# Kernel tuning notes

Measured on AMD Instinct MI355X. Metric: run time of the kernel, lower is better.

## Reference

```python
import jax, jax.numpy as jnp
import numpy as np

SIDE_LEN = 128
RESOLUTION = 1.0  # Angstrom per pixel


def setup_inputs() -> dict:
    key = jax.random.key(0)
    k1, k2, k3 = jax.random.split(key, 3)
    B, A = 16, 20000
    # atom xyz coords in Angstrom, spread within the field of view (+/- 63.5 A)
    mol = jax.random.normal(k1, (B, A, 3), dtype=jnp.float32) * 20.0
    # per-atom Gaussian std in [0.5, 1.5) A (strictly positive)
    stds = jax.random.uniform(k2, (A,), dtype=jnp.float32) + 0.5
    # per-atom density (mass) in [0.5, 1.5)
    densities = jax.random.uniform(k3, (A,), dtype=jnp.float32) + 0.5
    return {"mol": mol, "stds": stds, "densities": densities}


def reference(mol, stds, densities):
    # Pixel-center coordinate grid, identical to torch.arange(-x_max, x_max+1e-5, res)
    x_max = (SIDE_LEN - 1) * RESOLUTION / 2
    coord = jnp.arange(-x_max, x_max + 1e-5, RESOLUTION, dtype=jnp.float32)  # (S,)
    var = stds * stds                              # (A,)
    neg_half_inv_var = (-0.5 / var)[None, :, None] # (1,A,1)
    # Separable Gaussian profiles: exp(-(coord - mu)^2 / (2 var))
    dx = coord[None, None, :] - mol[:, :, 0:1]     # (B,A,S) x-offsets
    dy = coord[None, None, :] - mol[:, :, 1:2]     # (B,A,S) y-offsets
    gx = jnp.exp(neg_half_inv_var * dx * dx)       # (B,A,W)
    gy = jnp.exp(neg_half_inv_var * dy * dy)       # (B,A,H)
    coef = densities / (2.0 * jnp.pi * var)        # (A,)
    # img[b,h,w] = sum_a coef_a * gy[b,a,h] * gx[b,a,w]  (batched matmul)
    img = jnp.einsum('bah,baw->bhw', gy * coef[None, :, None], gx)
    return img  # (B, SIDE_LEN, SIDE_LEN)
```

## Files before the change

### kernel.cpp

```cpp
#include <hip/hip_runtime.h>


#define S 128
#define NS 32
#define PER 640
#define BLOCK 256

typedef _Float16 f16;
typedef _Float16 f16x2 __attribute__((ext_vector_type(2)));
typedef _Float16 f16x8 __attribute__((ext_vector_type(8)));
typedef float floatx16 __attribute__((ext_vector_type(16)));
typedef float floatx4 __attribute__((ext_vector_type(4)));

#if __has_builtin(__builtin_amdgcn_exp2f)
#define FAST_EXP2(x) __builtin_amdgcn_exp2f(x)
#else
#define FAST_EXP2(x) exp2f(x)
#endif
#if __has_builtin(__builtin_amdgcn_rcpf)
#define FAST_RCP(x) __builtin_amdgcn_rcpf(x)
#else
#define FAST_RCP(x) (1.0f / (x))
#endif

static __device__ __forceinline__ f16x2 PKRTZ(float a, float b) {
#if __has_builtin(__builtin_amdgcn_cvt_pkrtz)
    return __builtin_bit_cast(f16x2, __builtin_amdgcn_cvt_pkrtz(a, b));
#else
    return (f16x2){(f16)a, (f16)b};
#endif
}

union frag_u { f16x8 v; f16x2 h[4]; };

__global__ __launch_bounds__(BLOCK, 2) void k_proj(
    const float* __restrict__ mol,
    const float* __restrict__ stds,
    const float* __restrict__ dens,
    f16* __restrict__ part,
    int B, int A)
{
    __shared__ float4 sP[PER];

    const int ks   = blockIdx.x;
    const int b    = blockIdx.y;
    const int tid  = threadIdx.x;
    const int lane = tid & 63;
    const int wav  = tid >> 6;
    const int l31  = lane & 31;
    const int hi   = lane >> 5;

    const int a0  = ks * PER;
    const int a1  = min(a0 + PER, A);
    const int cnt = a1 - a0;

    for (int i = tid; i < cnt; i += BLOCK) {
        const int a = a0 + i;
        const size_t idx = (size_t)b * A + a;
        float x  = mol[idx * 3 + 0];
        float y  = mol[idx * 3 + 1];
        float v  = stds[a] * stds[a];
        float rv = FAST_RCP(v);
        sP[i] = make_float4(x, y, -0.72134752044448f * rv,
                            __log2f(dens[a] * 0.15915494309189535f * rv));
    }
    __syncthreads();

    const float py0 = (float)((wav >> 1) * 64 + l31) - 63.5f;
    const float px0 = (float)((wav & 1) * 64 + l31) - 63.5f;

    floatx16 acc00 = {0.f}, acc01 = {0.f}, acc10 = {0.f}, acc11 = {0.f};

    const int nk = cnt >> 4;
    const float4* sp = sP + hi * 8;

    auto kstep = [&](const float4 (&pp)[8]) {
        frag_u A0, A1, B0, B1;
#pragma unroll
        for (int jp = 0; jp < 4; ++jp) {
            float ea0[2], ea1[2], eb0[2], eb1[2];
#pragma unroll
            for (int u = 0; u < 2; ++u) {
                float4 p = pp[2 * jp + u];
                float dy = py0 - p.y;
                float t  = p.z * dy;
                float g0 = fmaf(t, dy, p.w);
                float g1 = fmaf(1024.0f, p.z, fmaf(64.0f, t, g0));
                ea0[u] = FAST_EXP2(g0);
                ea1[u] = FAST_EXP2(g1);
                float dx = px0 - p.x;
                float s  = p.z * dx;
                float h0 = s * dx;
                float h1 = fmaf(1024.0f, p.z, fmaf(64.0f, s, h0));
                eb0[u] = FAST_EXP2(h0);
                eb1[u] = FAST_EXP2(h1);
            }
            A0.h[jp] = PKRTZ(ea0[0], ea0[1]);
            A1.h[jp] = PKRTZ(ea1[0], ea1[1]);
            B0.h[jp] = PKRTZ(eb0[0], eb0[1]);
            B1.h[jp] = PKRTZ(eb1[0], eb1[1]);
        }
        acc00 = __builtin_amdgcn_mfma_f32_32x32x16_f16(A0.v, B0.v, acc00, 0, 0, 0);
        acc01 = __builtin_amdgcn_mfma_f32_32x32x16_f16(A0.v, B1.v, acc01, 0, 0, 0);
        acc10 = __builtin_amdgcn_mfma_f32_32x32x16_f16(A1.v, B0.v, acc10, 0, 0, 0);
        acc11 = __builtin_amdgcn_mfma_f32_32x32x16_f16(A1.v, B1.v, acc11, 0, 0, 0);
    };

    float4 c[8], n[8];
#pragma unroll
    for (int j = 0; j < 8; ++j) c[j] = sp[j];
    for (int s = 0; s < nk; s += 2) {
        const float4* sp1 = sp + (size_t)(s + 1) * 16;
#pragma unroll
        for (int j = 0; j < 8; ++j) n[j] = sp1[j];
        kstep(c);
        if (s + 2 < nk) {
            const float4* sp2 = sp + (size_t)(s + 2) * 16;
#pragma unroll
            for (int j = 0; j < 8; ++j) c[j] = sp2[j];
        }
        kstep(n);
    }

    f16* base = part + ((size_t)(b * NS + ks)) * (S * S) + (wav * 4) * 1024 + lane * 16;
    floatx16 accs[4] = {acc00, acc01, acc10, acc11};
#pragma unroll
    for (int q = 0; q < 4; ++q) {
        frag_u lo, hiv;
#pragma unroll
        for (int jp = 0; jp < 4; ++jp) {
            lo.h[jp]  = PKRTZ(accs[q][2 * jp],     accs[q][2 * jp + 1]);
            hiv.h[jp] = PKRTZ(accs[q][2 * jp + 8], accs[q][2 * jp + 9]);
        }
        *(f16x8*)(base + q * 1024 + 0) = lo.v;
        *(f16x8*)(base + q * 1024 + 8) = hiv.v;
    }
}

__global__ __launch_bounds__(256) void k_reduce(const f16* __restrict__ part,
                                                float* __restrict__ out) {
    const int b  = blockIdx.z;
    const int f8 = (blockIdx.x * 256 + threadIdx.x) * 8;

    const f16* src = part + (size_t)b * NS * (S * S) + f8;
    float sum[8] = {0.f};
    for (int s = 0; s < NS; ++s) {
        f16x8 v = *(const f16x8*)&src[(size_t)s * (S * S)];
#pragma unroll
        for (int i = 0; i < 8; ++i) sum[i] += (float)v[i];
    }

    const int reg0 = f8 & 15;
    const int lane = (f8 >> 4) & 63;
    const int q    = (f8 >> 10) & 3;
    const int w    = f8 >> 12;
    const int rowb = (w >> 1) * 64 + (q >> 1) * 32 + 4 * (lane >> 5);
    const int col  = (w & 1) * 64 + (q & 1) * 32 + (lane & 31);
#pragma unroll
    for (int i = 0; i < 8; ++i) {
        const int reg = reg0 + i;
        const int row = rowb + (reg & 3) + 8 * (reg >> 2);
        out[((size_t)b * S + row) * S + col] = sum[i];
    }
}

extern "C" void kernel_launch(void* const* d_in, const int* in_sizes, int n_in,
                              void* d_out, int out_size, void* d_ws, size_t ws_size,
                              hipStream_t stream) {
    const float* mol  = (const float*)d_in[0];
    const float* stds = (const float*)d_in[1];
    const float* dens = (const float*)d_in[2];
    float* out = (float*)d_out;

    const int A = in_sizes[1];
    const int B = in_sizes[0] / (A * 3);

    f16* part = (f16*)d_ws;

    k_proj<<<dim3(NS, B), dim3(BLOCK), 0, stream>>>(mol, stds, dens, part, B, A);
    k_reduce<<<dim3((S * S) / (256 * 8), 1, B), dim3(256), 0, stream>>>(part, out);
}
```

Baseline: 94.33 us.

## Use 2-wave blocks with 4x2 MFMA tiles per wave and finer atom split

Each wave now computes a full 128-row by 64-column strip using 4 y-fragments and 2 x-fragments, so 6 exp vectors feed 8 MFMAs instead of 4 feeding 4. This cuts exp work per output and cuts redundant y-profile computation. Blocks shrink to 128 threads and the atom dimension is split into 63 chunks of 320 to keep the grid large. In exchange the partial-sum buffer roughly doubles, making the reduce kernel read more, and accumulator register pressure rises. The reduce loop is unrolled by two and its index mapping is updated for the new tile layout.

Result: slower. 98.94 us (+4.9%).

```diff
diff --git a/kernel.cpp b/kernel.cpp
--- a/kernel.cpp
+++ b/kernel.cpp
@@ -2,15 +2,14 @@
 
 
 #define S 128
-#define NS 32
-#define PER 640
-#define BLOCK 256
+#define NS 63
+#define PER 320
+#define BLOCK 128
 
 typedef _Float16 f16;
 typedef _Float16 f16x2 __attribute__((ext_vector_type(2)));
 typedef _Float16 f16x8 __attribute__((ext_vector_type(8)));
 typedef float floatx16 __attribute__((ext_vector_type(16)));
-typedef float floatx4 __attribute__((ext_vector_type(4)));
 
 #if __has_builtin(__builtin_amdgcn_exp2f)
 #define FAST_EXP2(x) __builtin_amdgcn_exp2f(x)
@@ -66,28 +65,36 @@
     }
     __syncthreads();
 
-    const float py0 = (float)((wav >> 1) * 64 + l31) - 63.5f;
-    const float px0 = (float)((wav & 1) * 64 + l31) - 63.5f;
-
-    floatx16 acc00 = {0.f}, acc01 = {0.f}, acc10 = {0.f}, acc11 = {0.f};
+    const float py0 = (float)l31 - 63.5f;
+    const float px0 = (float)(wav * 64 + l31) - 63.5f;
+
+    floatx16 acc[4][2];
+#pragma unroll
+    for (int r = 0; r < 4; ++r)
+#pragma unroll
+        for (int cb = 0; cb < 2; ++cb) acc[r][cb] = (floatx16){0.f};
 
     const int nk = cnt >> 4;
     const float4* sp = sP + hi * 8;
 
     auto kstep = [&](const float4 (&pp)[8]) {
-        frag_u A0, A1, B0, B1;
+        frag_u A0, A1, A2, A3, B0, B1;
 #pragma unroll
         for (int jp = 0; jp < 4; ++jp) {
-            float ea0[2], ea1[2], eb0[2], eb1[2];
+            float ea0[2], ea1[2], ea2[2], ea3[2], eb0[2], eb1[2];
 #pragma unroll
             for (int u = 0; u < 2; ++u) {
                 float4 p = pp[2 * jp + u];
                 float dy = py0 - p.y;
                 float t  = p.z * dy;
                 float g0 = fmaf(t, dy, p.w);
-                float g1 = fmaf(1024.0f, p.z, fmaf(64.0f, t, g0));
+                float g1 = fmaf(1024.0f, p.z, fmaf( 64.0f, t, g0));
+                float g2 = fmaf(4096.0f, p.z, fmaf(128.0f, t, g0));
+                float g3 = fmaf(9216.0f, p.z, fmaf(192.0f, t, g0));
                 ea0[u] = FAST_EXP2(g0);
                 ea1[u] = FAST_EXP2(g1);
+                ea2[u] = FAST_EXP2(g2);
+                ea3[u] = FAST_EXP2(g3);
                 float dx = px0 - p.x;
                 float s  = p.z * dx;
                 float h0 = s * dx;
@@ -97,13 +104,19 @@
             }
             A0.h[jp] = PKRTZ(ea0[0], ea0[1]);
             A1.h[jp] = PKRTZ(ea1[0], ea1[1]);
+            A2.h[jp] = PKRTZ(ea2[0], ea2[1]);
+            A3.h[jp] = PKRTZ(ea3[0], ea3[1]);
             B0.h[jp] = PKRTZ(eb0[0], eb0[1]);
             B1.h[jp] = PKRTZ(eb1[0], eb1[1]);
         }
-        acc00 = __builtin_amdgcn_mfma_f32_32x32x16_f16(A0.v, B0.v, acc00, 0, 0, 0);
-        acc01 = __builtin_amdgcn_mfma_f32_32x32x16_f16(A0.v, B1.v, acc01, 0, 0, 0);
-        acc10 = __builtin_amdgcn_mfma_f32_32x32x16_f16(A1.v, B0.v, acc10, 0, 0, 0);
-        acc11 = __builtin_amdgcn_mfma_f32_32x32x16_f16(A1.v, B1.v, acc11, 0, 0, 0);
+        acc[0][0] = __builtin_amdgcn_mfma_f32_32x32x16_f16(A0.v, B0.v, acc[0][0], 0, 0, 0);
+        acc[0][1] = __builtin_amdgcn_mfma_f32_32x32x16_f16(A0.v, B1.v, acc[0][1], 0, 0, 0);
+        acc[1][0] = __builtin_amdgcn_mfma_f32_32x32x16_f16(A1.v, B0.v, acc[1][0], 0, 0, 0);
+        acc[1][1] = __builtin_amdgcn_mfma_f32_32x32x16_f16(A1.v, B1.v, acc[1][1], 0, 0, 0);
+        acc[2][0] = __builtin_amdgcn_mfma_f32_32x32x16_f16(A2.v, B0.v, acc[2][0], 0, 0, 0);
+        acc[2][1] = __builtin_amdgcn_mfma_f32_32x32x16_f16(A2.v, B1.v, acc[2][1], 0, 0, 0);
+        acc[3][0] = __builtin_amdgcn_mfma_f32_32x32x16_f16(A3.v, B0.v, acc[3][0], 0, 0, 0);
+        acc[3][1] = __builtin_amdgcn_mfma_f32_32x32x16_f16(A3.v, B1.v, acc[3][1], 0, 0, 0);
     };
 
     float4 c[8], n[8];
@@ -122,18 +135,21 @@
         kstep(n);
     }
 
-    f16* base = part + ((size_t)(b * NS + ks)) * (S * S) + (wav * 4) * 1024 + lane * 16;
-    floatx16 accs[4] = {acc00, acc01, acc10, acc11};
-#pragma unroll
-    for (int q = 0; q < 4; ++q) {
-        frag_u lo, hiv;
-#pragma unroll
-        for (int jp = 0; jp < 4; ++jp) {
-            lo.h[jp]  = PKRTZ(accs[q][2 * jp],     accs[q][2 * jp + 1]);
-            hiv.h[jp] = PKRTZ(accs[q][2 * jp + 8], accs[q][2 * jp + 9]);
+    f16* base = part + ((size_t)(b * NS + ks)) * (S * S) + lane * 16;
+#pragma unroll
+    for (int r = 0; r < 4; ++r) {
+#pragma unroll
+        for (int cb = 0; cb < 2; ++cb) {
+            f16* pq = base + (size_t)(r * 4 + (wav * 2 + cb)) * 1024;
+            frag_u lo, hiv;
+#pragma unroll
+            for (int jp = 0; jp < 4; ++jp) {
+                lo.h[jp]  = PKRTZ(acc[r][cb][2 * jp],     acc[r][cb][2 * jp + 1]);
+                hiv.h[jp] = PKRTZ(acc[r][cb][2 * jp + 8], acc[r][cb][2 * jp + 9]);
+            }
+            *(f16x8*)(pq + 0) = lo.v;
+            *(f16x8*)(pq + 8) = hiv.v;
         }
-        *(f16x8*)(base + q * 1024 + 0) = lo.v;
-        *(f16x8*)(base + q * 1024 + 8) = hiv.v;
     }
 }
 
@@ -143,24 +159,32 @@
     const int f8 = (blockIdx.x * 256 + threadIdx.x) * 8;
 
     const f16* src = part + (size_t)b * NS * (S * S) + f8;
-    float sum[8] = {0.f};
-    for (int s = 0; s < NS; ++s) {
-        f16x8 v = *(const f16x8*)&src[(size_t)s * (S * S)];
-#pragma unroll
-        for (int i = 0; i < 8; ++i) sum[i] += (float)v[i];
+    float s0[8] = {0.f}, s1[8] = {0.f};
+    int s = 0;
+    for (; s + 1 < NS; s += 2) {
+        f16x8 v0 = *(const f16x8*)&src[(size_t)s * (S * S)];
+        f16x8 v1 = *(const f16x8*)&src[(size_t)(s + 1) * (S * S)];
+#pragma unroll
+        for (int i = 0; i < 8; ++i) { s0[i] += (float)v0[i]; s1[i] += (float)v1[i]; }
+    }
+    if (s < NS) {
+        f16x8 v0 = *(const f16x8*)&src[(size_t)s * (S * S)];
+#pragma unroll
+        for (int i = 0; i < 8; ++i) s0[i] += (float)v0[i];
     }
 
     const int reg0 = f8 & 15;
     const int lane = (f8 >> 4) & 63;
-    const int q    = (f8 >> 10) & 3;
-    const int w    = f8 >> 12;
-    const int rowb = (w >> 1) * 64 + (q >> 1) * 32 + 4 * (lane >> 5);
-    const int col  = (w & 1) * 64 + (q & 1) * 32 + (lane & 31);
+    const int tile = f8 >> 10;
+    const int r    = tile >> 2;
+    const int cc   = tile & 3;
+    const int rowb = r * 32 + 4 * (lane >> 5);
+    const int col  = cc * 32 + (lane & 31);
 #pragma unroll
     for (int i = 0; i < 8; ++i) {
         const int reg = reg0 + i;
         const int row = rowb + (reg & 3) + 8 * (reg >> 2);
-        out[((size_t)b * S + row) * S + col] = sum[i];
+        out[((size_t)b * S + row) * S + col] = s0[i] + s1[i];
     }
 }
 
```

## Split image rows across two blocks to double grid and occupancy

Applied to the files above, without the earlier changes.

The projection kernel now splits the 128 output rows into two halves across a new grid dimension. Each wave computes a 64x32 strip with two MFMA accumulators instead of a 64x64 tile with four. The grid doubles and occupancy is raised to 4 blocks per SIMD group, while the per-block register footprint shrinks. In exchange, the x-profile exps are still computed per half, so exp work per output rises (3 exps per 2 MFMAs vs 4 per 4), and the atom staging into LDS is done twice. The register double-buffering is also removed, and the reduce kernel uses two accumulators with a new tile indexing.

After: 103.8 us. 1.1x slower.

```diff
diff --git a/kernel.cpp b/kernel.cpp
--- a/kernel.cpp
+++ b/kernel.cpp
@@ -4,13 +4,13 @@
 #define S 128
 #define NS 32
 #define PER 640
+#define QS 2
 #define BLOCK 256
 
 typedef _Float16 f16;
 typedef _Float16 f16x2 __attribute__((ext_vector_type(2)));
 typedef _Float16 f16x8 __attribute__((ext_vector_type(8)));
 typedef float floatx16 __attribute__((ext_vector_type(16)));
-typedef float floatx4 __attribute__((ext_vector_type(4)));
 
 #if __has_builtin(__builtin_amdgcn_exp2f)
 #define FAST_EXP2(x) __builtin_amdgcn_exp2f(x)
@@ -33,7 +33,7 @@
 
 union frag_u { f16x8 v; f16x2 h[4]; };
 
-__global__ __launch_bounds__(BLOCK, 2) void k_proj(
+__global__ __launch_bounds__(BLOCK, 4) void k_proj(
     const float* __restrict__ mol,
     const float* __restrict__ stds,
     const float* __restrict__ dens,
@@ -43,7 +43,8 @@
     __shared__ float4 sP[PER];
 
     const int ks   = blockIdx.x;
-    const int b    = blockIdx.y;
+    const int q    = blockIdx.y;
+    const int b    = blockIdx.z;
     const int tid  = threadIdx.x;
     const int lane = tid & 63;
     const int wav  = tid >> 6;
@@ -66,19 +67,20 @@
     }
     __syncthreads();
 
-    const float py0 = (float)((wav >> 1) * 64 + l31) - 63.5f;
-    const float px0 = (float)((wav & 1) * 64 + l31) - 63.5f;
+    const float py0 = (float)(q * 64 + l31) - 63.5f;
+    const float px0 = (float)(wav * 32 + l31) - 63.5f;
 
-    floatx16 acc00 = {0.f}, acc01 = {0.f}, acc10 = {0.f}, acc11 = {0.f};
+    floatx16 acc0 = {0.f}, acc1 = {0.f};
 
     const int nk = cnt >> 4;
     const float4* sp = sP + hi * 8;
 
-    auto kstep = [&](const float4 (&pp)[8]) {
-        frag_u A0, A1, B0, B1;
+    for (int s = 0; s < nk; ++s) {
+        const float4* pp = sp + (size_t)s * 16;
+        frag_u A0, A1, B0;
 #pragma unroll
         for (int jp = 0; jp < 4; ++jp) {
-            float ea0[2], ea1[2], eb0[2], eb1[2];
+            float ea0[2], ea1[2], eb0[2];
 #pragma unroll
             for (int u = 0; u < 2; ++u) {
                 float4 p = pp[2 * jp + u];
@@ -89,51 +91,29 @@
                 ea0[u] = FAST_EXP2(g0);
                 ea1[u] = FAST_EXP2(g1);
                 float dx = px0 - p.x;
-                float s  = p.z * dx;
-                float h0 = s * dx;
-                float h1 = fmaf(1024.0f, p.z, fmaf(64.0f, s, h0));
-                eb0[u] = FAST_EXP2(h0);
-                eb1[u] = FAST_EXP2(h1);
+                eb0[u] = FAST_EXP2((p.z * dx) * dx);
             }
             A0.h[jp] = PKRTZ(ea0[0], ea0[1]);
             A1.h[jp] = PKRTZ(ea1[0], ea1[1]);
             B0.h[jp] = PKRTZ(eb0[0], eb0[1]);
-            B1.h[jp] = PKRTZ(eb1[0], eb1[1]);
         }
-        acc00 = __builtin_amdgcn_mfma_f32_32x32x16_f16(A0.v, B0.v, acc00, 0, 0, 0);
-        acc01 = __builtin_amdgcn_mfma_f32_32x32x16_f16(A0.v, B1.v, acc01, 0, 0, 0);
-        acc10 = __builtin_amdgcn_mfma_f32_32x32x16_f16(A1.v, B0.v, acc10, 0, 0, 0);
-        acc11 = __builtin_amdgcn_mfma_f32_32x32x16_f16(A1.v, B1.v, acc11, 0, 0, 0);
-    };
-
-    float4 c[8], n[8];
-#pragma unroll
-    for (int j = 0; j < 8; ++j) c[j] = sp[j];
-    for (int s = 0; s < nk; s += 2) {
-        const float4* sp1 = sp + (size_t)(s + 1) * 16;
-#pragma unroll
-        for (int j = 0; j < 8; ++j) n[j] = sp1[j];
-        kstep(c);
-        if (s + 2 < nk) {
-            const float4* sp2 = sp + (size_t)(s + 2) * 16;
-#pragma unroll
-            for (int j = 0; j < 8; ++j) c[j] = sp2[j];
-        }
-        kstep(n);
+        acc0 = __builtin_amdgcn_mfma_f32_32x32x16_f16(A0.v, B0.v, acc0, 0, 0, 0);
+        acc1 = __builtin_amdgcn_mfma_f32_32x32x16_f16(A1.v, B0.v, acc1, 0, 0, 0);
     }
 
-    f16* base = part + ((size_t)(b * NS + ks)) * (S * S) + (wav * 4) * 1024 + lane * 16;
-    floatx16 accs[4] = {acc00, acc01, acc10, acc11};
+    f16* base = part + ((size_t)(b * NS + ks)) * (S * S) + lane * 16;
+    floatx16 accs[2] = {acc0, acc1};
 #pragma unroll
-    for (int q = 0; q < 4; ++q) {
+    for (int rr = 0; rr < 2; ++rr) {
+        f16* pq = base + (size_t)((q * 2 + rr) * 4 + wav) * 1024;
         frag_u lo, hiv;
 #pragma unroll
         for (int jp = 0; jp < 4; ++jp) {
-            lo.h[jp]  = PKRTZ(accs[q][2 * jp],     accs[q][2 * jp + 1]);
-            hiv.h[jp] = PKRTZ(accs[q][2 * jp + 8], accs[q][2 * jp + 9]);
+            lo.h[jp]  = PKRTZ(accs[rr][2 * jp],     accs[rr][2 * jp + 1]);
+            hiv.h[jp] = PKRTZ(accs[rr][2 * jp + 8], accs[rr][2 * jp + 9]);
         }
-        *(f16x8*)(base + q * 1024 + 0) = lo.v;
-        *(f16x8*)(base + q * 1024 + 8) = hiv.v;
+        *(f16x8*)(pq + 0) = lo.v;
+        *(f16x8*)(pq + 8) = hiv.v;
     }
 }
 
@@ -143,24 +123,26 @@
     const int f8 = (blockIdx.x * 256 + threadIdx.x) * 8;
 
     const f16* src = part + (size_t)b * NS * (S * S) + f8;
-    float sum[8] = {0.f};
-    for (int s = 0; s < NS; ++s) {
-        f16x8 v = *(const f16x8*)&src[(size_t)s * (S * S)];
+    float s0[8] = {0.f}, s1[8] = {0.f};
+    for (int s = 0; s < NS; s += 2) {
+        f16x8 v0 = *(const f16x8*)&src[(size_t)s * (S * S)];
+        f16x8 v1 = *(const f16x8*)&src[(size_t)(s + 1) * (S * S)];
 #pragma unroll
-        for (int i = 0; i < 8; ++i) sum[i] += (float)v[i];
+        for (int i = 0; i < 8; ++i) { s0[i] += (float)v0[i]; s1[i] += (float)v1[i]; }
     }
 
     const int reg0 = f8 & 15;
     const int lane = (f8 >> 4) & 63;
-    const int q    = (f8 >> 10) & 3;
-    const int w    = f8 >> 12;
-    const int rowb = (w >> 1) * 64 + (q >> 1) * 32 + 4 * (lane >> 5);
-    const int col  = (w & 1) * 64 + (q & 1) * 32 + (lane & 31);
+    const int tile = f8 >> 10;
+    const int r    = tile >> 2;
+    const int cc   = tile & 3;
+    const int rowb = r * 32 + 4 * (lane >> 5);
+    const int col  = cc * 32 + (lane & 31);
 #pragma unroll
     for (int i = 0; i < 8; ++i) {
         const int reg = reg0 + i;
         const int row = rowb + (reg & 3) + 8 * (reg >> 2);
-        out[((size_t)b * S + row) * S + col] = sum[i];
+        out[((size_t)b * S + row) * S + col] = s0[i] + s1[i];
     }
 }
 
@@ -177,6 +159,6 @@
 
     f16* part = (f16*)d_ws;
 
-    k_proj<<<dim3(NS, B), dim3(BLOCK), 0, stream>>>(mol, stds, dens, part, B, A);
+    k_proj<<<dim3(NS, QS, B), dim3(BLOCK), 0, stream>>>(mol, stds, dens, part, B, A);
     k_reduce<<<dim3((S * S) / (256 * 8), 1, B), dim3(256), 0, stream>>>(part, out);
 }
```
